# Kernel tuning notes

Hardware: AMD Instinct MI355X
Metric: run time of the kernel (lower is better)

Reference implementation:

```python
import jax, jax.numpy as jnp
import numpy as np
from jax import lax

K = 3  # kernel size
CO = 64  # out_channels
CI = 64  # in_channels


def setup_inputs() -> dict:
    key = jax.random.key(0)
    k1, k2, k3, k4, k5 = jax.random.split(key, 5)
    x = jax.random.normal(k1, (16, CI, 128, 128), dtype=jnp.float32)
    w1 = jax.random.normal(k2, (2 * CI, 32), dtype=jnp.float32) * 0.05
    b1 = jax.random.normal(k3, (32,), dtype=jnp.float32) * 0.05
    w2 = jax.random.normal(k4, (32, CO * CI * K * K), dtype=jnp.float32) * 0.05
    b2 = jax.random.normal(k5, (CO * CI * K * K,), dtype=jnp.float32) * 0.05
    return {"x": x, "w1": w1, "b1": b1, "w2": w2, "b2": b2}


def reference(x, w1, b1, w2, b2):
    B = x.shape[0]
    # per-sample channel statistics over spatial dims (torch.std is unbiased, ddof=1)
    mean = jnp.mean(x, axis=(2, 3))                      # [B, CI]
    std = jnp.std(x, axis=(2, 3), ddof=1)                # [B, CI]
    stats = jnp.concatenate([mean, std], axis=-1)        # [B, 2*CI]
    h = jax.nn.relu(stats @ w1 + b1)                     # [B, 32]
    kernels = (h @ w2 + b2).reshape(B, CO, CI, K, K)     # per-sample conv kernels

    def conv_one(xi, wi):
        # xi: [CI,H,W], wi: [CO,CI,K,K]; stride=1, padding=1, no bias
        return lax.conv_general_dilated(
            xi[None], wi, window_strides=(1, 1), padding=[(1, 1), (1, 1)],
            dimension_numbers=("NCHW", "OIHW", "NCHW"))[0]

    return jax.vmap(conv_one)(x, kernels)                # [B, CO, H, W]
```

## Files before the change

### kernel.cpp

```cpp
#include <hip/hip_runtime.h>
#include <hip/hip_bf16.h>


#define B_ 16
#define NPIX 16384
#define KEL 36864
#define XT_RS 8320

typedef __attribute__((ext_vector_type(4))) float f32x4;
typedef __attribute__((ext_vector_type(8))) short short8;

static __device__ __forceinline__ short bf16_of(float f) {
    __hip_bfloat16 h = __float2bfloat16(f);
    return *reinterpret_cast<short*>(&h);
}

__global__ __launch_bounds__(256) void xpose_stats(const float* __restrict__ x,
                                                   short* __restrict__ xT,
                                                   float* __restrict__ part) {
    int b = blockIdx.x, cig = blockIdx.y, pt = blockIdx.z;
    int t = threadIdx.x;
    int y = pt * 8 + (t >> 5);
    int x0 = (t & 31) * 4;

    const float* xb = x + ((size_t)(b * 64 + cig * 8)) * NPIX;
    short* xTb = xT + (size_t)b * 128 * XT_RS;

    float s[8], ss[8];
    f32x4 v[8];
    #pragma unroll
    for (int c = 0; c < 8; c++) {
        v[c] = *(const f32x4*)(xb + (size_t)c * NPIX + y * 128 + x0);
        s[c]  = v[c][0] + v[c][1] + v[c][2] + v[c][3];
        ss[c] = v[c][0]*v[c][0] + v[c][1]*v[c][1] + v[c][2]*v[c][2] + v[c][3]*v[c][3];
    }
    #pragma unroll
    for (int xi = 0; xi < 4; xi++) {
        short8 o;
        #pragma unroll
        for (int c = 0; c < 8; c++) o[c] = bf16_of(v[c][xi]);
        *(short8*)(xTb + ((size_t)(y * 130 + x0 + xi + 1)) * 64 + cig * 8) = o;
    }
    if (t < 16) {
        int y2 = pt * 8 + (t & 7);
        int col = (t & 8) ? 129 : 0;
        short8 z = {0, 0, 0, 0, 0, 0, 0, 0};
        *(short8*)(xTb + ((size_t)(y2 * 130 + col)) * 64 + cig * 8) = z;
    }

    __shared__ float red[4][16];
    int lane = t & 63, w = t >> 6;
    #pragma unroll
    for (int c = 0; c < 8; c++) {
        float a = s[c], q = ss[c];
        for (int off = 32; off; off >>= 1) { a += __shfl_down(a, off); q += __shfl_down(q, off); }
        if (lane == 0) { red[w][c * 2] = a; red[w][c * 2 + 1] = q; }
    }
    __syncthreads();
    if (t < 16)
        part[((size_t)((b * 8 + cig) * 16 + pt)) * 16 + t] =
            red[0][t] + red[1][t] + red[2][t] + red[3][t];
}

__global__ __launch_bounds__(256) void kern_gen(const float* __restrict__ part,
                                                const float* __restrict__ w1,
                                                const float* __restrict__ b1,
                                                const float* __restrict__ w2,
                                                const float* __restrict__ b2,
                                                short* __restrict__ wT) {
    __shared__ float st[16][128];
    __shared__ float hT[32][16];
    int t = threadIdx.x;

    for (int id = t; id < 1024; id += 256) {
        int b = id >> 6, ci = id & 63;
        const float* pb = part + ((size_t)((b * 8 + (ci >> 3)) * 16)) * 16 + (ci & 7) * 2;
        float s = 0.f, q = 0.f;
        #pragma unroll
        for (int p = 0; p < 16; p++) { s += pb[p * 16]; q += pb[p * 16 + 1]; }
        float mean = s * (1.f / NPIX);
        float var = fmaxf((q - s * mean) * (1.f / (NPIX - 1)), 0.f);
        st[b][ci] = mean;
        st[b][64 + ci] = sqrtf(var);
    }
    __syncthreads();
    for (int id = t; id < 512; id += 256) {
        int b = id >> 5, jj = id & 31;
        float acc = b1[jj];
        for (int i = 0; i < 128; i++) acc += st[b][i] * w1[i * 32 + jj];
        hT[jj][b] = fmaxf(acc, 0.f);
    }
    __syncthreads();

    int j = blockIdx.x * 256 + t;
    float wv[32];
    #pragma unroll
    for (int i = 0; i < 32; i++) wv[i] = w2[(size_t)i * KEL + j];
    float bv = b2[j];

    float acc[16];
    #pragma unroll
    for (int b = 0; b < 16; b++) acc[b] = bv;
    #pragma unroll
    for (int i = 0; i < 32; i++) {
        float wvi = wv[i];
        const f32x4* hr = (const f32x4*)&hT[i][0];
        #pragma unroll
        for (int q4 = 0; q4 < 4; q4++) {
            f32x4 hq = hr[q4];
            acc[q4 * 4 + 0] += hq[0] * wvi;
            acc[q4 * 4 + 1] += hq[1] * wvi;
            acc[q4 * 4 + 2] += hq[2] * wvi;
            acc[q4 * 4 + 3] += hq[3] * wvi;
        }
    }

    int co = j / 576;
    int rem = j - co * 576;
    int ci = rem / 9;
    int tap = rem - ci * 9;
    size_t dst = (size_t)tap * 4096 + co * 64 + ((((ci >> 3) ^ (co & 7)) << 3) | (ci & 7));
    #pragma unroll
    for (int b = 0; b < 16; b++)
        wT[(size_t)b * KEL + dst] = bf16_of(acc[b]);
}

__global__ __launch_bounds__(512, 2) void conv_mfma(const short* __restrict__ xT,
                                                    const short* __restrict__ wT,
                                                    float* __restrict__ out) {
    __shared__ __align__(16) short xls[10 * 528 * 8];
    __shared__ __align__(16) short wls[9 * 512 * 8];

    int b = blockIdx.x, xt = blockIdx.y, ytg = blockIdx.z;
    int x0 = xt * 64, Y0 = ytg * 16;
    int t = threadIdx.x;
    int l = t & 63, w = t >> 6;
    int ch = w & 1, r = w >> 1;
    int l15 = l & 15, lg = l >> 4;

    const short* xTb = xT + (size_t)b * 128 * XT_RS;
    const short* wTb = wT + (size_t)b * KEL;

#define ZROW(sl_)                                                              \
    {   short8 z8 = {0, 0, 0, 0, 0, 0, 0, 0};                                  \
        for (int e = t; e < 528; e += 512)                                     \
            *(short8*)(xls + ((sl_) * 528 + e) * 8) = z8; }

#define DMAROW(sl_, y_)                                                        \
    {   _Pragma("unroll")                                                      \
        for (int it = 0; it < 2; it++) {                                       \
            int e = it * 512 + t;                                              \
            if (e < 528) {                                                     \
                int xi = e >> 3, s = e & 7;                                    \
                const short* src = xTb + (size_t)(y_) * XT_RS                  \
                    + (x0 + xi) * 64 + ((s ^ (xi & 7)) << 3);                  \
                __builtin_amdgcn_global_load_lds(                              \
                    (const __attribute__((address_space(1))) void*)src,        \
                    (__attribute__((address_space(3))) void*)                   \
                        (xls + ((sl_) * 528 + it * 512 + (t & ~63)) * 8),      \
                    16, 0, 0);                                                 \
            }                                                                  \
        } }

    #pragma unroll
    for (int it = 0; it < 9; it++) {
        int e = it * 512 + t;
        __builtin_amdgcn_global_load_lds(
            (const __attribute__((address_space(1))) void*)(wTb + (size_t)e * 8),
            (__attribute__((address_space(3))) void*)(wls + (it * 512 + (t & ~63)) * 8),
            16, 0, 0);
    }
    #pragma unroll
    for (int k = 0; k < 6; k++) {
        int y = Y0 - 1 + k;
        if (y < 0) { ZROW(k); } else { DMAROW(k, y); }
    }
    asm volatile("s_waitcnt vmcnt(0)" ::: "memory");
    __syncthreads();

    int rbase = 0;
    #pragma unroll 1
    for (int j = 0; j < 4; j++) {
        if (j < 3) {
            #pragma unroll
            for (int m = 0; m < 4; m++) {
                int sl = rbase + 6 + m; if (sl >= 10) sl -= 10;
                int y = Y0 + 4 * j + 5 + m;
                if (y > 127) { ZROW(sl); } else { DMAROW(sl, y); }
            }
        }

        int y0 = Y0 + 4 * j;
        f32x4 acc[4][2];
        #pragma unroll
        for (int n = 0; n < 4; n++)
            #pragma unroll
            for (int g = 0; g < 2; g++) acc[n][g] = (f32x4){0.f, 0.f, 0.f, 0.f};

        #pragma unroll
        for (int kp = 0; kp < 2; kp++) {
            int sig = kp * 4 + lg;
            int pa = sig ^ (l15 & 7);
            #pragma unroll
            for (int tap = 0; tap < 9; tap++) {
                const int dy = tap / 3, dx = tap % 3;
                int sl = rbase + r + dy; if (sl >= 10) sl -= 10;
                short8 a0 = *(const short8*)&wls[(tap * 512 + (ch * 32 + l15) * 8 + pa) * 8];
                short8 a1 = *(const short8*)&wls[(tap * 512 + (ch * 32 + 16 + l15) * 8 + pa) * 8];
                #pragma unroll
                for (int n = 0; n < 4; n++) {
                    int xi = n * 16 + l15 + dx;
                    short8 bf = *(const short8*)&xls[(sl * 528 + xi * 8 + (sig ^ (xi & 7))) * 8];
                    acc[n][0] = __builtin_amdgcn_mfma_f32_16x16x32_bf16(a0, bf, acc[n][0], 0, 0, 0);
                    acc[n][1] = __builtin_amdgcn_mfma_f32_16x16x32_bf16(a1, bf, acc[n][1], 0, 0, 0);
                }
            }
        }

        #pragma unroll
        for (int g = 0; g < 2; g++) {
            float* ob = out + ((size_t)(b * 64 + ch * 32 + g * 16 + lg * 4)) * NPIX
                            + (y0 + r) * 128 + x0 + l15;
            #pragma unroll
            for (int reg = 0; reg < 4; reg++)
                #pragma unroll
                for (int n = 0; n < 4; n++)
                    ob[(size_t)reg * NPIX + n * 16] = acc[n][g][reg];
        }

        if (j < 3) {
            asm volatile("s_waitcnt vmcnt(0)" ::: "memory");
            __syncthreads();
        }
        rbase += 4; if (rbase >= 10) rbase -= 10;
    }
#undef ZROW
#undef DMAROW
}

extern "C" void kernel_launch(void* const* d_in, const int* in_sizes, int n_in,
                              void* d_out, int out_size, void* d_ws, size_t ws_size,
                              hipStream_t stream) {
    const float* x  = (const float*)d_in[0];
    const float* w1 = (const float*)d_in[1];
    const float* b1 = (const float*)d_in[2];
    const float* w2 = (const float*)d_in[3];
    const float* b2 = (const float*)d_in[4];
    float* out = (float*)d_out;

    float* part = (float*)d_ws;
    short* wT = (short*)((char*)d_ws + 131072);
    short* xT = (short*)((char*)d_ws + 131072 + 1179648);

    xpose_stats<<<dim3(B_, 8, 16), 256, 0, stream>>>(x, xT, part);
    kern_gen<<<dim3(144), 256, 0, stream>>>(part, w1, b1, w2, b2, wT);
    conv_mfma<<<dim3(B_, 2, 8), 512, 0, stream>>>(xT, wT, out);
}
```

Measured before the change: 64.78 us.

## Retile conv kernel to 8-row blocks with 4x4 MFMA register tiles per wave

The conv kernel now handles 8 output rows per block instead of 16, loading all 10 halo rows up front rather than streaming them through a ring buffer. Each wave computes a 4-row by 16-column by 64-channel tile, so every loaded A and B fragment feeds four MFMAs instead of two. The grid doubles to 512 blocks and launch bounds drop to one block per CU. In exchange the kernel gives up overlap between row loads and compute, re-reads more halo rows (10 for 8 output rows), and uses more accumulator registers.

```diff
diff --git a/kernel.cpp b/kernel.cpp
--- a/kernel.cpp
+++ b/kernel.cpp
@@ -125,42 +125,21 @@
         wT[(size_t)b * KEL + dst] = bf16_of(acc[b]);
 }
 
-__global__ __launch_bounds__(512, 2) void conv_mfma(const short* __restrict__ xT,
+__global__ __launch_bounds__(512, 1) void conv_mfma(const short* __restrict__ xT,
                                                     const short* __restrict__ wT,
                                                     float* __restrict__ out) {
     __shared__ __align__(16) short xls[10 * 528 * 8];
     __shared__ __align__(16) short wls[9 * 512 * 8];
 
-    int b = blockIdx.x, xt = blockIdx.y, ytg = blockIdx.z;
-    int x0 = xt * 64, Y0 = ytg * 16;
+    int b = blockIdx.x, xt = blockIdx.y, yo = blockIdx.z;
+    int x0 = xt * 64, y0 = yo * 8;
     int t = threadIdx.x;
     int l = t & 63, w = t >> 6;
-    int ch = w & 1, r = w >> 1;
+    int xq = w & 3, rh = w >> 2;
     int l15 = l & 15, lg = l >> 4;
 
     const short* xTb = xT + (size_t)b * 128 * XT_RS;
     const short* wTb = wT + (size_t)b * KEL;
-
-#define ZROW(sl_)                                                              \
-    {   short8 z8 = {0, 0, 0, 0, 0, 0, 0, 0};                                  \
-        for (int e = t; e < 528; e += 512)                                     \
-            *(short8*)(xls + ((sl_) * 528 + e) * 8) = z8; }
-
-#define DMAROW(sl_, y_)                                                        \
-    {   _Pragma("unroll")                                                      \
-        for (int it = 0; it < 2; it++) {                                       \
-            int e = it * 512 + t;                                              \
-            if (e < 528) {                                                     \
-                int xi = e >> 3, s = e & 7;                                    \
-                const short* src = xTb + (size_t)(y_) * XT_RS                  \
-                    + (x0 + xi) * 64 + ((s ^ (xi & 7)) << 3);                  \
-                __builtin_amdgcn_global_load_lds(                              \
-                    (const __attribute__((address_space(1))) void*)src,        \
-                    (__attribute__((address_space(3))) void*)                   \
-                        (xls + ((sl_) * 528 + it * 512 + (t & ~63)) * 8),      \
-                    16, 0, 0);                                                 \
-            }                                                                  \
-        } }
 
     #pragma unroll
     for (int it = 0; it < 9; it++) {
@@ -171,71 +150,73 @@
             16, 0, 0);
     }
     #pragma unroll
-    for (int k = 0; k < 6; k++) {
-        int y = Y0 - 1 + k;
-        if (y < 0) { ZROW(k); } else { DMAROW(k, y); }
-    }
-    asm volatile("s_waitcnt vmcnt(0)" ::: "memory");
-    __syncthreads();
-
-    int rbase = 0;
-    #pragma unroll 1
-    for (int j = 0; j < 4; j++) {
-        if (j < 3) {
-            #pragma unroll
-            for (int m = 0; m < 4; m++) {
-                int sl = rbase + 6 + m; if (sl >= 10) sl -= 10;
-                int y = Y0 + 4 * j + 5 + m;
-                if (y > 127) { ZROW(sl); } else { DMAROW(sl, y); }
-            }
-        }
-
-        int y0 = Y0 + 4 * j;
-        f32x4 acc[4][2];
-        #pragma unroll
-        for (int n = 0; n < 4; n++)
-            #pragma unroll
-            for (int g = 0; g < 2; g++) acc[n][g] = (f32x4){0.f, 0.f, 0.f, 0.f};
-
-        #pragma unroll
-        for (int kp = 0; kp < 2; kp++) {
-            int sig = kp * 4 + lg;
-            int pa = sig ^ (l15 & 7);
-            #pragma unroll
-            for (int tap = 0; tap < 9; tap++) {
-                const int dy = tap / 3, dx = tap % 3;
-                int sl = rbase + r + dy; if (sl >= 10) sl -= 10;
-                short8 a0 = *(const short8*)&wls[(tap * 512 + (ch * 32 + l15) * 8 + pa) * 8];
-                short8 a1 = *(const short8*)&wls[(tap * 512 + (ch * 32 + 16 + l15) * 8 + pa) * 8];
-                #pragma unroll
-                for (int n = 0; n < 4; n++) {
-                    int xi = n * 16 + l15 + dx;
-                    short8 bf = *(const short8*)&xls[(sl * 528 + xi * 8 + (sig ^ (xi & 7))) * 8];
-                    acc[n][0] = __builtin_amdgcn_mfma_f32_16x16x32_bf16(a0, bf, acc[n][0], 0, 0, 0);
-                    acc[n][1] = __builtin_amdgcn_mfma_f32_16x16x32_bf16(a1, bf, acc[n][1], 0, 0, 0);
+    for (int lr = 0; lr < 10; lr++) {
+        int y = y0 - 1 + lr;
+        if (y < 0 || y > 127) {
+            short8 z8 = {0, 0, 0, 0, 0, 0, 0, 0};
+            for (int e = t; e < 528; e += 512)
+                *(short8*)(xls + (lr * 528 + e) * 8) = z8;
+        } else {
+            #pragma unroll
+            for (int it = 0; it < 2; it++) {
+                int e = it * 512 + t;
+                if (e < 528) {
+                    int xi = e >> 3, s = e & 7;
+                    const short* src = xTb + (size_t)y * XT_RS
+                        + (x0 + xi) * 64 + ((s ^ (xi & 7)) << 3);
+                    __builtin_amdgcn_global_load_lds(
+                        (const __attribute__((address_space(1))) void*)src,
+                        (__attribute__((address_space(3))) void*)
+                            (xls + (lr * 528 + it * 512 + (t & ~63)) * 8),
+                        16, 0, 0);
                 }
             }
         }
-
-        #pragma unroll
-        for (int g = 0; g < 2; g++) {
-            float* ob = out + ((size_t)(b * 64 + ch * 32 + g * 16 + lg * 4)) * NPIX
-                            + (y0 + r) * 128 + x0 + l15;
-            #pragma unroll
-            for (int reg = 0; reg < 4; reg++)
+    }
+    asm volatile("s_waitcnt vmcnt(0) lgkmcnt(0)" ::: "memory");
+    __builtin_amdgcn_s_barrier();
+    __builtin_amdgcn_sched_barrier(0);
+
+    f32x4 acc[4][4];
+    #pragma unroll
+    for (int r = 0; r < 4; r++)
+        #pragma unroll
+        for (int g = 0; g < 4; g++) acc[r][g] = (f32x4){0.f, 0.f, 0.f, 0.f};
+
+    #pragma unroll
+    for (int kp = 0; kp < 2; kp++) {
+        int sig = kp * 4 + lg;
+        int pa = sig ^ (l15 & 7);
+        #pragma unroll
+        for (int tap = 0; tap < 9; tap++) {
+            const int dy = tap / 3, dx = tap % 3;
+            short8 a[4], bf[4];
+            #pragma unroll
+            for (int g = 0; g < 4; g++)
+                a[g] = *(const short8*)&wls[(tap * 512 + (g * 16 + l15) * 8 + pa) * 8];
+            int xi = xq * 16 + l15 + dx;
+            int sw = sig ^ (xi & 7);
+            #pragma unroll
+            for (int r = 0; r < 4; r++)
+                bf[r] = *(const short8*)&xls[((rh * 4 + r + dy) * 528 + xi * 8 + sw) * 8];
+            #pragma unroll
+            for (int r = 0; r < 4; r++)
                 #pragma unroll
-                for (int n = 0; n < 4; n++)
-                    ob[(size_t)reg * NPIX + n * 16] = acc[n][g][reg];
+                for (int g = 0; g < 4; g++)
+                    acc[r][g] = __builtin_amdgcn_mfma_f32_16x16x32_bf16(a[g], bf[r], acc[r][g], 0, 0, 0);
         }
-
-        if (j < 3) {
-            asm volatile("s_waitcnt vmcnt(0)" ::: "memory");
-            __syncthreads();
-        }
-        rbase += 4; if (rbase >= 10) rbase -= 10;
-    }
-#undef ZROW
-#undef DMAROW
+    }
+
+    #pragma unroll
+    for (int g = 0; g < 4; g++) {
+        float* ob = out + ((size_t)(b * 64 + g * 16 + lg * 4)) * NPIX
+                        + (y0 + rh * 4) * 128 + x0 + xq * 16 + l15;
+        #pragma unroll
+        for (int reg = 0; reg < 4; reg++)
+            #pragma unroll
+            for (int r = 0; r < 4; r++)
+                ob[(size_t)reg * NPIX + r * 128] = acc[r][g][reg];
+    }
 }
 
 extern "C" void kernel_launch(void* const* d_in, const int* in_sizes, int n_in,
@@ -254,5 +235,5 @@
 
     xpose_stats<<<dim3(B_, 8, 16), 256, 0, stream>>>(x, xT, part);
     kern_gen<<<dim3(144), 256, 0, stream>>>(part, w1, b1, w2, b2, wT);
-    conv_mfma<<<dim3(B_, 2, 8), 512, 0, stream>>>(xT, wT, out);
-}
+    conv_mfma<<<dim3(B_, 2, 16), 512, 0, stream>>>(xT, wT, out);
+}
```

Result: slower. 66.40 us (+2.5%).

## Fuse stats, kernel generation and conv into one persistent kernel with grid barriers

Applied to the files above, without the earlier changes.

Merges the three launches (transpose+stats, per-sample kernel generation, MFMA conv) into a single 256-block kernel that uses atomic-counter grid barriers between phases. Each block now covers half the rows of an 8-channel group in the first phase, and the kernel-gen phase runs on 72 blocks of 512 threads. The aim is to remove launch gaps and inter-kernel drain/fill costs. It adds a memset of the counter and relies on all 256 blocks being co-resident. It also gives up the conv's two-blocks-per-CU occupancy hint.

```diff
diff --git a/kernel.cpp b/kernel.cpp
--- a/kernel.cpp
+++ b/kernel.cpp
@@ -15,131 +15,155 @@
     return *reinterpret_cast<short*>(&h);
 }
 
-__global__ __launch_bounds__(256) void xpose_stats(const float* __restrict__ x,
-                                                   short* __restrict__ xT,
-                                                   float* __restrict__ part) {
-    int b = blockIdx.x, cig = blockIdx.y, pt = blockIdx.z;
+static __device__ __forceinline__ void grid_barrier(unsigned* cnt, unsigned tgt) {
+    __syncthreads();
+    __threadfence();
+    if (threadIdx.x == 0) {
+        __hip_atomic_fetch_add(cnt, 1u, __ATOMIC_ACQ_REL, __HIP_MEMORY_SCOPE_AGENT);
+        while (__hip_atomic_load(cnt, __ATOMIC_ACQUIRE, __HIP_MEMORY_SCOPE_AGENT) < tgt)
+            __builtin_amdgcn_s_sleep(2);
+    }
+    __syncthreads();
+    __threadfence();
+}
+
+__global__ __launch_bounds__(512) void fused(const float* __restrict__ x,
+                                             const float* __restrict__ w1,
+                                             const float* __restrict__ b1,
+                                             const float* __restrict__ w2,
+                                             const float* __restrict__ b2,
+                                             unsigned* cnt,
+                                             float* __restrict__ part,
+                                             short* __restrict__ wT,
+                                             short* __restrict__ xT,
+                                             float* __restrict__ out) {
+    __shared__ __align__(16) char smem[158208];
     int t = threadIdx.x;
-    int y = pt * 8 + (t >> 5);
-    int x0 = (t & 31) * 4;
-
-    const float* xb = x + ((size_t)(b * 64 + cig * 8)) * NPIX;
-    short* xTb = xT + (size_t)b * 128 * XT_RS;
-
-    float s[8], ss[8];
-    f32x4 v[8];
-    #pragma unroll
-    for (int c = 0; c < 8; c++) {
-        v[c] = *(const f32x4*)(xb + (size_t)c * NPIX + y * 128 + x0);
-        s[c]  = v[c][0] + v[c][1] + v[c][2] + v[c][3];
-        ss[c] = v[c][0]*v[c][0] + v[c][1]*v[c][1] + v[c][2]*v[c][2] + v[c][3]*v[c][3];
-    }
-    #pragma unroll
-    for (int xi = 0; xi < 4; xi++) {
-        short8 o;
-        #pragma unroll
-        for (int c = 0; c < 8; c++) o[c] = bf16_of(v[c][xi]);
-        *(short8*)(xTb + ((size_t)(y * 130 + x0 + xi + 1)) * 64 + cig * 8) = o;
-    }
-    if (t < 16) {
-        int y2 = pt * 8 + (t & 7);
-        int col = (t & 8) ? 129 : 0;
-        short8 z = {0, 0, 0, 0, 0, 0, 0, 0};
-        *(short8*)(xTb + ((size_t)(y2 * 130 + col)) * 64 + cig * 8) = z;
-    }
-
-    __shared__ float red[4][16];
-    int lane = t & 63, w = t >> 6;
-    #pragma unroll
-    for (int c = 0; c < 8; c++) {
-        float a = s[c], q = ss[c];
-        for (int off = 32; off; off >>= 1) { a += __shfl_down(a, off); q += __shfl_down(q, off); }
-        if (lane == 0) { red[w][c * 2] = a; red[w][c * 2 + 1] = q; }
-    }
-    __syncthreads();
-    if (t < 16)
-        part[((size_t)((b * 8 + cig) * 16 + pt)) * 16 + t] =
-            red[0][t] + red[1][t] + red[2][t] + red[3][t];
-}
-
-__global__ __launch_bounds__(256) void kern_gen(const float* __restrict__ part,
-                                                const float* __restrict__ w1,
-                                                const float* __restrict__ b1,
-                                                const float* __restrict__ w2,
-                                                const float* __restrict__ b2,
-                                                short* __restrict__ wT) {
-    __shared__ float st[16][128];
-    __shared__ float hT[32][16];
-    int t = threadIdx.x;
-
-    for (int id = t; id < 1024; id += 256) {
-        int b = id >> 6, ci = id & 63;
-        const float* pb = part + ((size_t)((b * 8 + (ci >> 3)) * 16)) * 16 + (ci & 7) * 2;
-        float s = 0.f, q = 0.f;
-        #pragma unroll
-        for (int p = 0; p < 16; p++) { s += pb[p * 16]; q += pb[p * 16 + 1]; }
-        float mean = s * (1.f / NPIX);
-        float var = fmaxf((q - s * mean) * (1.f / (NPIX - 1)), 0.f);
-        st[b][ci] = mean;
-        st[b][64 + ci] = sqrtf(var);
-    }
-    __syncthreads();
-    for (int id = t; id < 512; id += 256) {
-        int b = id >> 5, jj = id & 31;
-        float acc = b1[jj];
-        for (int i = 0; i < 128; i++) acc += st[b][i] * w1[i * 32 + jj];
-        hT[jj][b] = fmaxf(acc, 0.f);
-    }
-    __syncthreads();
-
-    int j = blockIdx.x * 256 + t;
-    float wv[32];
-    #pragma unroll
-    for (int i = 0; i < 32; i++) wv[i] = w2[(size_t)i * KEL + j];
-    float bv = b2[j];
-
-    float acc[16];
-    #pragma unroll
-    for (int b = 0; b < 16; b++) acc[b] = bv;
-    #pragma unroll
-    for (int i = 0; i < 32; i++) {
-        float wvi = wv[i];
-        const f32x4* hr = (const f32x4*)&hT[i][0];
-        #pragma unroll
-        for (int q4 = 0; q4 < 4; q4++) {
-            f32x4 hq = hr[q4];
-            acc[q4 * 4 + 0] += hq[0] * wvi;
-            acc[q4 * 4 + 1] += hq[1] * wvi;
-            acc[q4 * 4 + 2] += hq[2] * wvi;
-            acc[q4 * 4 + 3] += hq[3] * wvi;
-        }
-    }
-
-    int co = j / 576;
-    int rem = j - co * 576;
-    int ci = rem / 9;
-    int tap = rem - ci * 9;
-    size_t dst = (size_t)tap * 4096 + co * 64 + ((((ci >> 3) ^ (co & 7)) << 3) | (ci & 7));
-    #pragma unroll
-    for (int b = 0; b < 16; b++)
-        wT[(size_t)b * KEL + dst] = bf16_of(acc[b]);
-}
-
-__global__ __launch_bounds__(512, 2) void conv_mfma(const short* __restrict__ xT,
-                                                    const short* __restrict__ wT,
-                                                    float* __restrict__ out) {
-    __shared__ __align__(16) short xls[10 * 528 * 8];
-    __shared__ __align__(16) short wls[9 * 512 * 8];
-
-    int b = blockIdx.x, xt = blockIdx.y, ytg = blockIdx.z;
-    int x0 = xt * 64, Y0 = ytg * 16;
-    int t = threadIdx.x;
-    int l = t & 63, w = t >> 6;
-    int ch = w & 1, r = w >> 1;
-    int l15 = l & 15, lg = l >> 4;
-
-    const short* xTb = xT + (size_t)b * 128 * XT_RS;
-    const short* wTb = wT + (size_t)b * KEL;
+    int blk = blockIdx.x;
+
+    {
+        int b = blk & 15, cig = (blk >> 4) & 7, half = blk >> 7;
+        const float* xb = x + ((size_t)(b * 64 + cig * 8)) * NPIX;
+        short* xTb = xT + (size_t)b * 128 * XT_RS;
+
+        float s[8], ss[8];
+        #pragma unroll
+        for (int c = 0; c < 8; c++) { s[c] = 0.f; ss[c] = 0.f; }
+        int yl = t >> 5, x0 = (t & 31) * 4;
+
+        #pragma unroll 1
+        for (int yo = 0; yo < 4; yo++) {
+            int y = half * 64 + yo * 16 + yl;
+            f32x4 v[8];
+            #pragma unroll
+            for (int c = 0; c < 8; c++) {
+                v[c] = *(const f32x4*)(xb + (size_t)c * NPIX + y * 128 + x0);
+                s[c]  += v[c][0] + v[c][1] + v[c][2] + v[c][3];
+                ss[c] += v[c][0]*v[c][0] + v[c][1]*v[c][1] + v[c][2]*v[c][2] + v[c][3]*v[c][3];
+            }
+            #pragma unroll
+            for (int xi = 0; xi < 4; xi++) {
+                short8 o;
+                #pragma unroll
+                for (int c = 0; c < 8; c++) o[c] = bf16_of(v[c][xi]);
+                *(short8*)(xTb + ((size_t)(y * 130 + x0 + xi + 1)) * 64 + cig * 8) = o;
+            }
+        }
+        if (t < 128) {
+            int y2 = half * 64 + (t & 63);
+            int col = (t >> 6) ? 129 : 0;
+            short8 z = {0, 0, 0, 0, 0, 0, 0, 0};
+            *(short8*)(xTb + ((size_t)(y2 * 130 + col)) * 64 + cig * 8) = z;
+        }
+
+        float* red = (float*)smem;
+        int lane = t & 63, w = t >> 6;
+        #pragma unroll
+        for (int c = 0; c < 8; c++) {
+            float a = s[c], q = ss[c];
+            for (int off = 32; off; off >>= 1) { a += __shfl_down(a, off); q += __shfl_down(q, off); }
+            if (lane == 0) { red[w * 16 + c * 2] = a; red[w * 16 + c * 2 + 1] = q; }
+        }
+        __syncthreads();
+        if (t < 16) {
+            float a = 0.f;
+            #pragma unroll
+            for (int w2i = 0; w2i < 8; w2i++) a += red[w2i * 16 + t];
+            part[(size_t)(b * 8 + cig) * 32 + half * 16 + t] = a;
+        }
+    }
+    grid_barrier(cnt, 256);
+
+    if (blk < 72) {
+        float* st = (float*)smem;
+        float* hT = (float*)(smem + 8192);
+        for (int id = t; id < 1024; id += 512) {
+            int b = id >> 6, ci = id & 63;
+            float s = 0.f, q = 0.f;
+            #pragma unroll
+            for (int hh = 0; hh < 2; hh++) {
+                const float* pb = part + (size_t)(b * 8 + (ci >> 3)) * 32 + hh * 16 + (ci & 7) * 2;
+                s += pb[0]; q += pb[1];
+            }
+            float mean = s * (1.f / NPIX);
+            float var = fmaxf((q - s * mean) * (1.f / (NPIX - 1)), 0.f);
+            st[b * 128 + ci] = mean;
+            st[b * 128 + 64 + ci] = sqrtf(var);
+        }
+        __syncthreads();
+        {
+            int b = t >> 5, jj = t & 31;
+            float acc = b1[jj];
+            for (int i = 0; i < 128; i++) acc += st[b * 128 + i] * w1[i * 32 + jj];
+            hT[jj * 16 + b] = fmaxf(acc, 0.f);
+        }
+        __syncthreads();
+
+        int j = blk * 512 + t;
+        float wv[32];
+        #pragma unroll
+        for (int i = 0; i < 32; i++) wv[i] = w2[(size_t)i * KEL + j];
+        float bv = b2[j];
+
+        float acc[16];
+        #pragma unroll
+        for (int b = 0; b < 16; b++) acc[b] = bv;
+        #pragma unroll
+        for (int i = 0; i < 32; i++) {
+            float wvi = wv[i];
+            const f32x4* hr = (const f32x4*)&hT[i * 16];
+            #pragma unroll
+            for (int q4 = 0; q4 < 4; q4++) {
+                f32x4 hq = hr[q4];
+                acc[q4 * 4 + 0] += hq[0] * wvi;
+                acc[q4 * 4 + 1] += hq[1] * wvi;
+                acc[q4 * 4 + 2] += hq[2] * wvi;
+                acc[q4 * 4 + 3] += hq[3] * wvi;
+            }
+        }
+        int co = j / 576;
+        int rem = j - co * 576;
+        int ci = rem / 9;
+        int tap = rem - ci * 9;
+        size_t dst = (size_t)tap * 4096 + co * 64 + ((((ci >> 3) ^ (co & 7)) << 3) | (ci & 7));
+        #pragma unroll
+        for (int b = 0; b < 16; b++)
+            wT[(size_t)b * KEL + dst] = bf16_of(acc[b]);
+    }
+    grid_barrier(cnt, 512);
+
+    {
+        short* xls = (short*)smem;
+        short* wls = (short*)(smem + 84480);
+
+        int b = blk & 15, xt = (blk >> 4) & 1, ytg = blk >> 5;
+        int x0 = xt * 64, Y0 = ytg * 16;
+        int l = t & 63, w = t >> 6;
+        int ch = w & 1, r = w >> 1;
+        int l15 = l & 15, lg = l >> 4;
+
+        const short* xTb = xT + (size_t)b * 128 * XT_RS;
+        const short* wTb = wT + (size_t)b * KEL;
 
 #define ZROW(sl_)                                                              \
     {   short8 z8 = {0, 0, 0, 0, 0, 0, 0, 0};                                  \
@@ -151,9 +175,9 @@
         for (int it = 0; it < 2; it++) {                                       \
             int e = it * 512 + t;                                              \
             if (e < 528) {                                                     \
-                int xi = e >> 3, s = e & 7;                                    \
+                int xi = e >> 3, sl8 = e & 7;                                  \
                 const short* src = xTb + (size_t)(y_) * XT_RS                  \
-                    + (x0 + xi) * 64 + ((s ^ (xi & 7)) << 3);                  \
+                    + (x0 + xi) * 64 + ((sl8 ^ (xi & 7)) << 3);                \
                 __builtin_amdgcn_global_load_lds(                              \
                     (const __attribute__((address_space(1))) void*)src,        \
                     (__attribute__((address_space(3))) void*)                   \
@@ -162,80 +186,81 @@
             }                                                                  \
         } }
 
-    #pragma unroll
-    for (int it = 0; it < 9; it++) {
-        int e = it * 512 + t;
-        __builtin_amdgcn_global_load_lds(
-            (const __attribute__((address_space(1))) void*)(wTb + (size_t)e * 8),
-            (__attribute__((address_space(3))) void*)(wls + (it * 512 + (t & ~63)) * 8),
-            16, 0, 0);
-    }
-    #pragma unroll
-    for (int k = 0; k < 6; k++) {
-        int y = Y0 - 1 + k;
-        if (y < 0) { ZROW(k); } else { DMAROW(k, y); }
-    }
-    asm volatile("s_waitcnt vmcnt(0)" ::: "memory");
-    __syncthreads();
-
-    int rbase = 0;
-    #pragma unroll 1
-    for (int j = 0; j < 4; j++) {
-        if (j < 3) {
-            #pragma unroll
-            for (int m = 0; m < 4; m++) {
-                int sl = rbase + 6 + m; if (sl >= 10) sl -= 10;
-                int y = Y0 + 4 * j + 5 + m;
-                if (y > 127) { ZROW(sl); } else { DMAROW(sl, y); }
-            }
-        }
-
-        int y0 = Y0 + 4 * j;
-        f32x4 acc[4][2];
-        #pragma unroll
-        for (int n = 0; n < 4; n++)
-            #pragma unroll
-            for (int g = 0; g < 2; g++) acc[n][g] = (f32x4){0.f, 0.f, 0.f, 0.f};
-
-        #pragma unroll
-        for (int kp = 0; kp < 2; kp++) {
-            int sig = kp * 4 + lg;
-            int pa = sig ^ (l15 & 7);
-            #pragma unroll
-            for (int tap = 0; tap < 9; tap++) {
-                const int dy = tap / 3, dx = tap % 3;
-                int sl = rbase + r + dy; if (sl >= 10) sl -= 10;
-                short8 a0 = *(const short8*)&wls[(tap * 512 + (ch * 32 + l15) * 8 + pa) * 8];
-                short8 a1 = *(const short8*)&wls[(tap * 512 + (ch * 32 + 16 + l15) * 8 + pa) * 8];
-                #pragma unroll
-                for (int n = 0; n < 4; n++) {
-                    int xi = n * 16 + l15 + dx;
-                    short8 bf = *(const short8*)&xls[(sl * 528 + xi * 8 + (sig ^ (xi & 7))) * 8];
-                    acc[n][0] = __builtin_amdgcn_mfma_f32_16x16x32_bf16(a0, bf, acc[n][0], 0, 0, 0);
-                    acc[n][1] = __builtin_amdgcn_mfma_f32_16x16x32_bf16(a1, bf, acc[n][1], 0, 0, 0);
+        #pragma unroll
+        for (int it = 0; it < 9; it++) {
+            int e = it * 512 + t;
+            __builtin_amdgcn_global_load_lds(
+                (const __attribute__((address_space(1))) void*)(wTb + (size_t)e * 8),
+                (__attribute__((address_space(3))) void*)(wls + (it * 512 + (t & ~63)) * 8),
+                16, 0, 0);
+        }
+        #pragma unroll
+        for (int k = 0; k < 6; k++) {
+            int y = Y0 - 1 + k;
+            if (y < 0) { ZROW(k); } else { DMAROW(k, y); }
+        }
+        asm volatile("s_waitcnt vmcnt(0)" ::: "memory");
+        __syncthreads();
+
+        int rbase = 0;
+        #pragma unroll 1
+        for (int j = 0; j < 4; j++) {
+            if (j < 3) {
+                #pragma unroll
+                for (int m = 0; m < 4; m++) {
+                    int sl = rbase + 6 + m; if (sl >= 10) sl -= 10;
+                    int y = Y0 + 4 * j + 5 + m;
+                    if (y > 127) { ZROW(sl); } else { DMAROW(sl, y); }
                 }
             }
-        }
-
-        #pragma unroll
-        for (int g = 0; g < 2; g++) {
-            float* ob = out + ((size_t)(b * 64 + ch * 32 + g * 16 + lg * 4)) * NPIX
-                            + (y0 + r) * 128 + x0 + l15;
-            #pragma unroll
-            for (int reg = 0; reg < 4; reg++)
-                #pragma unroll
-                for (int n = 0; n < 4; n++)
-                    ob[(size_t)reg * NPIX + n * 16] = acc[n][g][reg];
-        }
-
-        if (j < 3) {
-            asm volatile("s_waitcnt vmcnt(0)" ::: "memory");
-            __syncthreads();
-        }
-        rbase += 4; if (rbase >= 10) rbase -= 10;
-    }
+
+            int y0 = Y0 + 4 * j;
+            f32x4 acc[4][2];
+            #pragma unroll
+            for (int n = 0; n < 4; n++)
+                #pragma unroll
+                for (int g = 0; g < 2; g++) acc[n][g] = (f32x4){0.f, 0.f, 0.f, 0.f};
+
+            #pragma unroll
+            for (int kp = 0; kp < 2; kp++) {
+                int sig = kp * 4 + lg;
+                int pa = sig ^ (l15 & 7);
+                #pragma unroll
+                for (int tap = 0; tap < 9; tap++) {
+                    const int dy = tap / 3, dx = tap % 3;
+                    int sl = rbase + r + dy; if (sl >= 10) sl -= 10;
+                    short8 a0 = *(const short8*)&wls[(tap * 512 + (ch * 32 + l15) * 8 + pa) * 8];
+                    short8 a1 = *(const short8*)&wls[(tap * 512 + (ch * 32 + 16 + l15) * 8 + pa) * 8];
+                    #pragma unroll
+                    for (int n = 0; n < 4; n++) {
+                        int xi = n * 16 + l15 + dx;
+                        short8 bf = *(const short8*)&xls[(sl * 528 + xi * 8 + (sig ^ (xi & 7))) * 8];
+                        acc[n][0] = __builtin_amdgcn_mfma_f32_16x16x32_bf16(a0, bf, acc[n][0], 0, 0, 0);
+                        acc[n][1] = __builtin_amdgcn_mfma_f32_16x16x32_bf16(a1, bf, acc[n][1], 0, 0, 0);
+                    }
+                }
+            }
+
+            #pragma unroll
+            for (int g = 0; g < 2; g++) {
+                float* ob = out + ((size_t)(b * 64 + ch * 32 + g * 16 + lg * 4)) * NPIX
+                                + (y0 + r) * 128 + x0 + l15;
+                #pragma unroll
+                for (int reg = 0; reg < 4; reg++)
+                    #pragma unroll
+                    for (int n = 0; n < 4; n++)
+                        ob[(size_t)reg * NPIX + n * 16] = acc[n][g][reg];
+            }
+
+            if (j < 3) {
+                asm volatile("s_waitcnt vmcnt(0)" ::: "memory");
+                __syncthreads();
+            }
+            rbase += 4; if (rbase >= 10) rbase -= 10;
+        }
 #undef ZROW
 #undef DMAROW
+    }
 }
 
 extern "C" void kernel_launch(void* const* d_in, const int* in_sizes, int n_in,
@@ -248,11 +273,11 @@
     const float* b2 = (const float*)d_in[4];
     float* out = (float*)d_out;
 
-    float* part = (float*)d_ws;
-    short* wT = (short*)((char*)d_ws + 131072);
-    short* xT = (short*)((char*)d_ws + 131072 + 1179648);
-
-    xpose_stats<<<dim3(B_, 8, 16), 256, 0, stream>>>(x, xT, part);
-    kern_gen<<<dim3(144), 256, 0, stream>>>(part, w1, b1, w2, b2, wT);
-    conv_mfma<<<dim3(B_, 2, 8), 512, 0, stream>>>(xT, wT, out);
-}
+    unsigned* cnt = (unsigned*)d_ws;
+    float* part = (float*)((char*)d_ws + 4096);
+    short* wT = (short*)((char*)d_ws + 4096 + 16384);
+    short* xT = (short*)((char*)d_ws + 4096 + 16384 + 1179648);
+
+    hipMemsetAsync(d_ws, 0, 256, stream);
+    fused<<<dim3(256), dim3(512), 0, stream>>>(x, w1, b1, w2, b2, cnt, part, wT, xT, out);
+}
```

New measurement: 252.7 us. 290% more time.
